# Kernel optimization log

Measured on AMD Instinct MI355X. Metric: run time of the kernel, lower is better.

The kernel has to match this reference:

```python
import jax, jax.numpy as jnp
import numpy as np
import math

HEADS = 4
DIM_HEAD = 32
EPS = 1e-5

def _ln_channels(x):
    # LayerNorm over channel axis (axis=1) of NCHW, no affine (eps=1e-5)
    mu = jnp.mean(x, axis=1, keepdims=True)
    var = jnp.mean((x - mu) ** 2, axis=1, keepdims=True)
    return (x - mu) * jax.lax.rsqrt(var + EPS)

def setup_inputs() -> dict:
    key = jax.random.key(0)
    k1, k2, k3, k4 = jax.random.split(key, 4)
    dim, inner = 256, HEADS * DIM_HEAD
    x = jax.random.normal(k1, (16, dim, 64, 64), dtype=jnp.float32)
    Wqkv = jax.random.normal(k2, (3 * inner, dim), dtype=jnp.float32) * (1.0 / math.sqrt(dim))
    Wout = jax.random.normal(k3, (dim, inner), dtype=jnp.float32) * (1.0 / math.sqrt(inner))
    bout = jax.random.normal(k4, (dim,), dtype=jnp.float32) * 0.01
    return {"x": x, "Wqkv": Wqkv, "Wout": Wout, "bout": bout}

def reference(x, Wqkv, Wout, bout):
    B, C, H, W = x.shape
    N = H * W
    inner = HEADS * DIM_HEAD
    # pre-norm (channel-wise LayerNorm via permute in torch)
    normed = _ln_channels(x)
    # 1x1 conv to qkv: [B, 3*inner, H, W]
    qkv = jnp.einsum('oc,bchw->bohw', Wqkv, normed)
    q, k, v = jnp.split(qkv, 3, axis=1)
    # [B, inner, H, W] -> [B, heads, N, dim_head]
    def to_heads(t):
        return t.reshape(B, HEADS, DIM_HEAD, N).transpose(0, 1, 3, 2)
    q, k, v = to_heads(q), to_heads(k), to_heads(v)
    q = jax.nn.softmax(q, axis=-1)          # over dim_head
    k = jax.nn.softmax(k, axis=-2)          # over N
    q = q / math.sqrt(DIM_HEAD)
    v = v / N
    context = jnp.einsum('bhnd,bhne->bhde', k, v)   # [B,h,d,d]
    out = jnp.einsum('bhde,bhnd->bhne', context, q) # [B,h,N,d]
    out = out.transpose(0, 1, 3, 2).reshape(B, inner, H, W)
    out = jnp.einsum('oc,bchw->bohw', Wout, out) + bout[None, :, None, None]
    out = _ln_channels(out)                  # LinearAttention.out_norm
    return out + x                           # residual
```

## Files before the change

### kernel.cpp

```cpp
#include <hip/hip_runtime.h>
#include <hip/hip_bf16.h>
#include <math.h>

#define BATCH 16
#define CH 256
#define NPOS 4096
#define INNER 128
#define HEADS 4
#define DH 32

typedef __hip_bfloat16 bf16;
typedef short bf8v __attribute__((ext_vector_type(8)));
typedef float f32x4 __attribute__((ext_vector_type(4)));

__device__ __forceinline__ float b2f(bf16 v) { return __bfloat162float(v); }
__device__ __forceinline__ float us2f(unsigned short u) {
    unsigned w = ((unsigned)u) << 16; float f; __builtin_memcpy(&f, &w, 4); return f;
}
__device__ __forceinline__ unsigned short f2us(float f) {
    bf16 h = __float2bfloat16(f); unsigned short u; __builtin_memcpy(&u, &h, 2); return u;
}
__device__ __forceinline__ bf16 f2b(float v) { return __float2bfloat16(v); }

__global__ __launch_bounds__(256)
void prep_w_kernel(const float* __restrict__ Wqkv, bf16* __restrict__ wqb,
                   float* __restrict__ wqs) {
    int idx = (blockIdx.x * 256 + threadIdx.x) * 4;
    float4 w = *(const float4*)&Wqkv[idx];
    ushort4 u;
    u.x = f2us(w.x); u.y = f2us(w.y); u.z = f2us(w.z); u.w = f2us(w.w);
    *(ushort4*)&wqb[idx] = u;
    float s4 = us2f(u.x) + us2f(u.y) + us2f(u.z) + us2f(u.w);
    #pragma unroll
    for (int m = 1; m <= 32; m <<= 1) s4 += __shfl_xor(s4, m, 64);
    if ((threadIdx.x & 63) == 0)
        wqs[blockIdx.x * 4 + (threadIdx.x >> 6)] = s4;
}

__global__ __launch_bounds__(256)
void fused_qkv_kernel(const float* __restrict__ x, const bf16* __restrict__ wqb,
                      const float* __restrict__ wqs,
                      bf16* __restrict__ p, float* __restrict__ ctxp) {
    __shared__ char smem[36864];
    __shared__ float stats[640];

    const int b = blockIdx.y, tile = blockIdx.x, n0 = tile * 64;
    const int tid = threadIdx.x;
    const int w = tid >> 6, lane = tid & 63;
    const int lrow = lane & 15, kq = lane >> 4;
    bf16* A = (bf16*)smem;

    {
        const int nq = tid & 15, cp = tid >> 4;
        float s[4] = {0.f,0.f,0.f,0.f}, sq[4] = {0.f,0.f,0.f,0.f};
        #pragma unroll
        for (int i = 0; i < 8; ++i) {
            int c0 = cp * 2 + 32 * i;
            const float* xp = x + ((size_t)b * CH + c0) * NPOS + n0 + nq * 4;
            float4 fa = *(const float4*)xp;
            float4 fb = *(const float4*)(xp + NPOS);
            #pragma unroll
            for (int j = 0; j < 4; ++j) {
                float va = (&fa.x)[j], vb = (&fb.x)[j];
                s[j] += va + vb; sq[j] += va * va + vb * vb;
                *(unsigned*)&A[(nq * 4 + j) * 264 + c0] =
                    (unsigned)f2us(va) | ((unsigned)f2us(vb) << 16);
            }
        }
        #pragma unroll
        for (int j = 0; j < 4; ++j) {
            s[j]  += __shfl_xor(s[j], 16, 64);  sq[j] += __shfl_xor(sq[j], 16, 64);
            s[j]  += __shfl_xor(s[j], 32, 64);  sq[j] += __shfl_xor(sq[j], 32, 64);
            if (lane < 16) {
                stats[(nq * 4 + j) * 8 + w * 2]     = s[j];
                stats[(nq * 4 + j) * 8 + w * 2 + 1] = sq[j];
            }
        }
    }
    __syncthreads();
    if (tid < 64) {
        float s  = stats[tid*8] + stats[tid*8+2] + stats[tid*8+4] + stats[tid*8+6];
        float sq = stats[tid*8+1] + stats[tid*8+3] + stats[tid*8+5] + stats[tid*8+7];
        float m = s * (1.f / 256.f);
        float var = sq * (1.f / 256.f) - m * m;
        stats[512 + tid * 2] = m;
        stats[512 + tid * 2 + 1] = rsqrtf(var + 1e-5f);
    }
    __syncthreads();

    ushort4 ekp[4][2];
    float se0 = 0.f, se1 = 0.f;

    for (int ph = 0; ph < 3; ++ph) {
        const bf16* wp = wqb + (size_t)(ph * 128 + w * 32) * 256;
        const float cs0 = wqs[ph * 128 + w * 32 + lrow];
        const float cs1 = wqs[ph * 128 + w * 32 + 16 + lrow];
        f32x4 acc[4][2];
        #pragma unroll
        for (int i = 0; i < 4; ++i) {
            acc[i][0] = (f32x4){0.f,0.f,0.f,0.f};
            acc[i][1] = (f32x4){0.f,0.f,0.f,0.f};
        }
        #pragma unroll 4
        for (int k0 = 0; k0 < 256; k0 += 32) {
            bf8v af[4], bfr[2];
            #pragma unroll
            for (int t = 0; t < 4; ++t)
                af[t] = *(const bf8v*)&A[(t * 16 + lrow) * 264 + k0 + kq * 8];
            #pragma unroll
            for (int t = 0; t < 2; ++t)
                bfr[t] = *(const bf8v*)&wp[(size_t)(t * 16 + lrow) * 256 + k0 + kq * 8];
            #pragma unroll
            for (int mt = 0; mt < 4; ++mt)
                #pragma unroll
                for (int nt = 0; nt < 2; ++nt)
                    acc[mt][nt] = __builtin_amdgcn_mfma_f32_16x16x32_bf16(
                        af[mt], bfr[nt], acc[mt][nt], 0, 0, 0);
        }

        if (ph == 0) {
            unsigned* pg32 = (unsigned*)p;
            #pragma unroll
            for (int mt = 0; mt < 4; ++mt)
                #pragma unroll
                for (int r = 0; r < 4; ++r) {
                    int row = mt * 16 + kq * 4 + r;
                    float mu = stats[512 + row * 2], rsn = stats[512 + row * 2 + 1];
                    float e0 = __expf(b2f(f2b((acc[mt][0][r] - mu * cs0) * rsn)));
                    float e1 = __expf(b2f(f2b((acc[mt][1][r] - mu * cs1) * rsn)));
                    float s = e0 + e1;
                    s += __shfl_xor(s, 1, 64);  s += __shfl_xor(s, 2, 64);
                    s += __shfl_xor(s, 4, 64);  s += __shfl_xor(s, 8, 64);
                    float rd = 1.f / s;
                    pg32[(size_t)(b * NPOS + n0 + row) * 64 + w * 16 + lrow] =
                        (unsigned)f2us(e0 * rd) | ((unsigned)f2us(e1 * rd) << 16);
                }
        } else if (ph == 1) {
            se0 = 0.f; se1 = 0.f;
            #pragma unroll
            for (int mt = 0; mt < 4; ++mt) {
                ushort4 u0, u1;
                unsigned short q_;
                #pragma unroll
                for (int r = 0; r < 4; ++r) {
                    int row = mt * 16 + kq * 4 + r;
                    float mu = stats[512 + row * 2], rsn = stats[512 + row * 2 + 1];
                    q_ = f2us(__expf(b2f(f2b((acc[mt][0][r] - mu * cs0) * rsn))));
                    se0 += us2f(q_); (&u0.x)[r] = q_;
                    q_ = f2us(__expf(b2f(f2b((acc[mt][1][r] - mu * cs1) * rsn))));
                    se1 += us2f(q_); (&u1.x)[r] = q_;
                }
                ekp[mt][0] = u0; ekp[mt][1] = u1;
            }
            se0 += __shfl_xor(se0, 16, 64); se0 += __shfl_xor(se0, 32, 64);
            se1 += __shfl_xor(se1, 16, 64); se1 += __shfl_xor(se1, 32, 64);
        } else {
            __syncthreads();
            bf16* ekt = (bf16*)(smem + w * 9216);
            bf16* vt  = (bf16*)(smem + w * 9216 + 4608);
            #pragma unroll
            for (int mt = 0; mt < 4; ++mt)
                #pragma unroll
                for (int nt = 0; nt < 2; ++nt) {
                    float csx = nt ? cs1 : cs0;
                    ushort4 vv;
                    #pragma unroll
                    for (int r = 0; r < 4; ++r) {
                        int row = mt * 16 + kq * 4 + r;
                        float mu = stats[512 + row * 2], rsn = stats[512 + row * 2 + 1];
                        (&vv.x)[r] = f2us((acc[mt][nt][r] - mu * csx) * rsn);
                    }
                    int d = nt * 16 + lrow, n = mt * 16 + kq * 4;
                    *(ushort4*)&vt[d * 72 + n]  = vv;
                    *(ushort4*)&ekt[d * 72 + n] = ekp[mt][nt];
                }
            f32x4 cacc[2][2];
            cacc[0][0] = (f32x4){0.f,0.f,0.f,0.f}; cacc[0][1] = cacc[0][0];
            cacc[1][0] = cacc[0][0];               cacc[1][1] = cacc[0][0];
            #pragma unroll
            for (int ks = 0; ks < 2; ++ks) {
                bf8v a2[2], bv2[2];
                a2[0]  = *(const bf8v*)&ekt[lrow * 72 + ks * 32 + kq * 8];
                a2[1]  = *(const bf8v*)&ekt[(16 + lrow) * 72 + ks * 32 + kq * 8];
                bv2[0] = *(const bf8v*)&vt[lrow * 72 + ks * 32 + kq * 8];
                bv2[1] = *(const bf8v*)&vt[(16 + lrow) * 72 + ks * 32 + kq * 8];
                #pragma unroll
                for (int mt2 = 0; mt2 < 2; ++mt2)
                    #pragma unroll
                    for (int nt2 = 0; nt2 < 2; ++nt2)
                        cacc[mt2][nt2] = __builtin_amdgcn_mfma_f32_16x16x32_bf16(
                            a2[mt2], bv2[nt2], cacc[mt2][nt2], 0, 0, 0);
            }
            float* pb = ctxp + ((size_t)(b * 64 + tile) * 4 + w) * 1056;
            #pragma unroll
            for (int mt2 = 0; mt2 < 2; ++mt2)
                #pragma unroll
                for (int nt2 = 0; nt2 < 2; ++nt2)
                    #pragma unroll
                    for (int r = 0; r < 4; ++r) {
                        int d = mt2 * 16 + kq * 4 + r, e = nt2 * 16 + lrow;
                        pb[d * 32 + e] = cacc[mt2][nt2][r];
                    }
            if (kq == 0) {
                pb[1024 + lrow] = se0;
                pb[1024 + 16 + lrow] = se1;
            }
        }
    }
}

__global__ __launch_bounds__(256)
void ctx_wmod_kernel(const float* __restrict__ ctxp, const float* __restrict__ Wout,
                     bf16* __restrict__ wmod) {
    __shared__ float cs[1056];
    int h = blockIdx.x, b = blockIdx.y, ch = blockIdx.z;
    int tid = threadIdx.x;

    #pragma unroll
    for (int i = 0; i < 2; ++i) {
        int s = i * 256 + tid;
        if (s < 264) {
            f32x4 a = (f32x4){0.f,0.f,0.f,0.f};
            const float* src = ctxp + (size_t)(b * 64 * 4 + h) * 1056 + s * 4;
            for (int t = 0; t < 64; ++t)
                a += *(const f32x4*)(src + (size_t)t * 4 * 1056);
            *(f32x4*)&cs[s * 4] = a;
        }
    }
    __syncthreads();

    int c = ch * 128 + (tid >> 1);
    int dh = tid & 1;
    const float* wr = Wout + (size_t)c * INNER + h * DH;
    float wv[32];
    #pragma unroll
    for (int i = 0; i < 8; ++i) {
        float4 t = *(const float4*)&wr[i * 4];
        wv[i * 4] = t.x; wv[i * 4 + 1] = t.y; wv[i * 4 + 2] = t.z; wv[i * 4 + 3] = t.w;
    }
    const float SCALE = 4.3158341e-05f;
    unsigned* wm32 = (unsigned*)(wmod + ((size_t)b * CH + c) * INNER + h * DH);
    #pragma unroll
    for (int dd = 0; dd < 8; ++dd) {
        int d1 = dh * 8 + dd, d2 = d1 + 16;
        const float* c1 = &cs[d1 * 32];
        const float* c2 = &cs[d2 * 32];
        float s1 = 0.f, s2 = 0.f;
        #pragma unroll
        for (int e4 = 0; e4 < 8; ++e4) {
            f32x4 t1 = *(const f32x4*)&c1[e4 * 4];
            f32x4 t2 = *(const f32x4*)&c2[e4 * 4];
            #pragma unroll
            for (int j = 0; j < 4; ++j) {
                s1 += wv[e4 * 4 + j] * t1[j];
                s2 += wv[e4 * 4 + j] * t2[j];
            }
        }
        float v1 = s1 * SCALE / cs[1024 + d1];
        float v2 = s2 * SCALE / cs[1024 + d2];
        wm32[d1] = (unsigned)f2us(v1) | ((unsigned)f2us(v2) << 16);
    }
}

__global__ __launch_bounds__(256)
void fused_out_kernel(const bf16* __restrict__ p, const bf16* __restrict__ wmod,
                      const float* __restrict__ bout, const float* __restrict__ x,
                      float* __restrict__ out) {
    __shared__ char lds[37376];
    bf16* Ap = (bf16*)lds;
    float* ct = (float*)lds;
    float* st = (float*)(lds + 34816);

    const int b = blockIdx.y, n0 = blockIdx.x * 64;
    const int tid = threadIdx.x;
    const int w = tid >> 6, lane = tid & 63;
    const int lrow = lane & 15, kq = lane >> 4;

    {
        const uint4* pg = (const uint4*)p;
        unsigned* A32 = (unsigned*)Ap;
        #pragma unroll
        for (int i = 0; i < 4; ++i) {
            int idx = i * 256 + tid;
            int c4 = idx & 15, n = idx >> 4;
            uint4 u = pg[(size_t)(b * NPOS + n0 + n) * 16 + c4];
            *(uint4*)(A32 + n * 68 + c4 * 4) = u;
        }
    }
    __syncthreads();

    f32x4 acc[4][4];
    #pragma unroll
    for (int i = 0; i < 4; ++i)
        #pragma unroll
        for (int j = 0; j < 4; ++j) acc[i][j] = (f32x4){0.f, 0.f, 0.f, 0.f};

    const bf16* wb = wmod + (size_t)b * CH * INNER + (size_t)(w * 64) * INNER;
    #pragma unroll 2
    for (int k0 = 0; k0 < 128; k0 += 32) {
        bf8v af[4], bfr[4];
        #pragma unroll
        for (int t = 0; t < 4; ++t)
            af[t] = *(const bf8v*)&Ap[(t * 16 + lrow) * 136 + k0 + kq * 8];
        #pragma unroll
        for (int t = 0; t < 4; ++t)
            bfr[t] = *(const bf8v*)&wb[(size_t)(t * 16 + lrow) * 128 + k0 + kq * 8];
        #pragma unroll
        for (int mt = 0; mt < 4; ++mt)
            #pragma unroll
            for (int nt = 0; nt < 4; ++nt)
                acc[mt][nt] = __builtin_amdgcn_mfma_f32_16x16x32_bf16(
                    af[mt], bfr[nt], acc[mt][nt], 0, 0, 0);
    }

    #pragma unroll
    for (int nt = 0; nt < 4; ++nt) {
        float bv = bout[w * 64 + nt * 16 + lrow];
        #pragma unroll
        for (int mt = 0; mt < 4; ++mt)
            #pragma unroll
            for (int r = 0; r < 4; ++r) acc[mt][nt][r] += bv;
    }

    #pragma unroll
    for (int mt = 0; mt < 4; ++mt)
        #pragma unroll
        for (int r = 0; r < 4; ++r) {
            float s = 0.f, sq = 0.f;
            #pragma unroll
            for (int nt = 0; nt < 4; ++nt) {
                float v = acc[mt][nt][r];
                s += v; sq += v * v;
            }
            #pragma unroll
            for (int m = 1; m <= 8; m <<= 1) {
                s += __shfl_xor(s, m, 64);
                sq += __shfl_xor(sq, m, 64);
            }
            if (lrow == 0) {
                int row = mt * 16 + kq * 4 + r;
                st[w * 128 + row * 2] = s;
                st[w * 128 + row * 2 + 1] = sq;
            }
        }
    __syncthreads();
    if (tid < 64) {
        float s  = st[tid * 2]       + st[128 + tid * 2]
                 + st[256 + tid * 2] + st[384 + tid * 2];
        float sq = st[tid * 2 + 1]       + st[128 + tid * 2 + 1]
                 + st[256 + tid * 2 + 1] + st[384 + tid * 2 + 1];
        float m = s * (1.f / 256.f);
        float var = sq * (1.f / 256.f) - m * m;
        st[512 + tid * 2] = m;
        st[512 + tid * 2 + 1] = rsqrtf(var + 1e-5f);
    }
    __syncthreads();
    #pragma unroll
    for (int mt = 0; mt < 4; ++mt)
        #pragma unroll
        for (int r = 0; r < 4; ++r) {
            int row = mt * 16 + kq * 4 + r;
            float m = st[512 + row * 2], rs = st[512 + row * 2 + 1];
            #pragma unroll
            for (int nt = 0; nt < 4; ++nt)
                acc[mt][nt][r] = (acc[mt][nt][r] - m) * rs;
        }

    #pragma unroll 1
    for (int pr = 0; pr < 2; ++pr) {
        __syncthreads();
        if ((w >> 1) == pr) {
            #pragma unroll
            for (int mt = 0; mt < 4; ++mt)
                #pragma unroll
                for (int nt = 0; nt < 4; ++nt)
                    #pragma unroll
                    for (int r = 0; r < 4; ++r)
                        ct[((w & 1) * 64 + nt * 16 + lrow) * 68 + mt * 16 + kq * 4 + r]
                            = acc[mt][nt][r];
        }
        __syncthreads();
        #pragma unroll
        for (int i = 0; i < 8; ++i) {
            int idx = i * 256 + tid;
            int n4 = (idx & 15) * 4, cl = idx >> 4;
            size_t gi = ((size_t)b * CH + pr * 128 + cl) * NPOS + n0 + n4;
            f32x4 cv = *(const f32x4*)&ct[cl * 68 + n4];
            f32x4 xv = *(const f32x4*)&x[gi];
            __builtin_nontemporal_store(cv + xv, (f32x4*)&out[gi]);
        }
    }
}

extern "C" void kernel_launch(void* const* d_in, const int* in_sizes, int n_in,
                              void* d_out, int out_size, void* d_ws, size_t ws_size,
                              hipStream_t stream) {
    const float* x    = (const float*)d_in[0];
    const float* Wqkv = (const float*)d_in[1];
    const float* Wout = (const float*)d_in[2];
    const float* bout = (const float*)d_in[3];
    float* out = (float*)d_out;

    char* ws = (char*)d_ws;
    bf16*  p      = (bf16*)ws;
    float* ctxp   = (float*)(ws + 16777216);
    bf16*  wmod   = (bf16*)(ws + 34349056);
    bf16*  wqb    = (bf16*)(ws + 35397632);
    float* wqs    = (float*)(ws + 35594240);

    prep_w_kernel<<<dim3(96), 256, 0, stream>>>(Wqkv, wqb, wqs);
    fused_qkv_kernel<<<dim3(64, BATCH), 256, 0, stream>>>(x, wqb, wqs, p, ctxp);
    ctx_wmod_kernel<<<dim3(HEADS, BATCH, 2), 256, 0, stream>>>(ctxp, Wout, wmod);
    fused_out_kernel<<<dim3(64, BATCH), 256, 0, stream>>>(p, wmod, bout, x, out);
}
```

Measured before the change: 187.6 us.

## Recompute softmaxed Q in output kernel instead of round-tripping through global memory

Q is no longer computed and stored to a global bf16 buffer in the QKV kernel. Instead, the output kernel reloads x, converts it to bf16 in LDS, and recomputes the Q projection with MFMA using per-position LayerNorm mean/rstd that the first kernel saved. This removes the 16 MB write and read of Q. In exchange it adds a second 64 MB fp32 read of x and extra matmul and exp work in the output kernel.

Result: no change. 188.7 us (+0.6%).

```diff
diff --git a/kernel.cpp b/kernel.cpp
--- a/kernel.cpp
+++ b/kernel.cpp
@@ -39,8 +39,8 @@
 
 __global__ __launch_bounds__(256)
 void fused_qkv_kernel(const float* __restrict__ x, const bf16* __restrict__ wqb,
-                      const float* __restrict__ wqs,
-                      bf16* __restrict__ p, float* __restrict__ ctxp) {
+                      const float* __restrict__ wqs, float* __restrict__ musr,
+                      float* __restrict__ ctxp) {
     __shared__ char smem[36864];
     __shared__ float stats[640];
 
@@ -85,13 +85,15 @@
         float var = sq * (1.f / 256.f) - m * m;
         stats[512 + tid * 2] = m;
         stats[512 + tid * 2 + 1] = rsqrtf(var + 1e-5f);
+        float2 ms; ms.x = m; ms.y = stats[512 + tid * 2 + 1];
+        *(float2*)&musr[((size_t)b * NPOS + n0 + tid) * 2] = ms;
     }
     __syncthreads();
 
     ushort4 ekp[4][2];
     float se0 = 0.f, se1 = 0.f;
 
-    for (int ph = 0; ph < 3; ++ph) {
+    for (int ph = 1; ph < 3; ++ph) {
         const bf16* wp = wqb + (size_t)(ph * 128 + w * 32) * 256;
         const float cs0 = wqs[ph * 128 + w * 32 + lrow];
         const float cs1 = wqs[ph * 128 + w * 32 + 16 + lrow];
@@ -118,24 +120,7 @@
                         af[mt], bfr[nt], acc[mt][nt], 0, 0, 0);
         }
 
-        if (ph == 0) {
-            unsigned* pg32 = (unsigned*)p;
-            #pragma unroll
-            for (int mt = 0; mt < 4; ++mt)
-                #pragma unroll
-                for (int r = 0; r < 4; ++r) {
-                    int row = mt * 16 + kq * 4 + r;
-                    float mu = stats[512 + row * 2], rsn = stats[512 + row * 2 + 1];
-                    float e0 = __expf(b2f(f2b((acc[mt][0][r] - mu * cs0) * rsn)));
-                    float e1 = __expf(b2f(f2b((acc[mt][1][r] - mu * cs1) * rsn)));
-                    float s = e0 + e1;
-                    s += __shfl_xor(s, 1, 64);  s += __shfl_xor(s, 2, 64);
-                    s += __shfl_xor(s, 4, 64);  s += __shfl_xor(s, 8, 64);
-                    float rd = 1.f / s;
-                    pg32[(size_t)(b * NPOS + n0 + row) * 64 + w * 16 + lrow] =
-                        (unsigned)f2us(e0 * rd) | ((unsigned)f2us(e1 * rd) << 16);
-                }
-        } else if (ph == 1) {
+        if (ph == 1) {
             se0 = 0.f; se1 = 0.f;
             #pragma unroll
             for (int mt = 0; mt < 4; ++mt) {
@@ -263,10 +248,13 @@
 }
 
 __global__ __launch_bounds__(256)
-void fused_out_kernel(const bf16* __restrict__ p, const bf16* __restrict__ wmod,
+void fused_out_kernel(const bf16* __restrict__ wqb, const float* __restrict__ wqs,
+                      const float* __restrict__ musr, const bf16* __restrict__ wmod,
                       const float* __restrict__ bout, const float* __restrict__ x,
                       float* __restrict__ out) {
     __shared__ char lds[37376];
+    bf16* A  = (bf16*)lds;
+    float* mus = (float*)(lds + 33792);
     bf16* Ap = (bf16*)lds;
     float* ct = (float*)lds;
     float* st = (float*)(lds + 34816);
@@ -277,15 +265,77 @@
     const int lrow = lane & 15, kq = lane >> 4;
 
     {
-        const uint4* pg = (const uint4*)p;
-        unsigned* A32 = (unsigned*)Ap;
+        const int nq = tid & 15, cp = tid >> 4;
+        #pragma unroll
+        for (int i = 0; i < 8; ++i) {
+            int c0 = cp * 2 + 32 * i;
+            const float* xp = x + ((size_t)b * CH + c0) * NPOS + n0 + nq * 4;
+            float4 fa = *(const float4*)xp;
+            float4 fb = *(const float4*)(xp + NPOS);
+            #pragma unroll
+            for (int j = 0; j < 4; ++j)
+                *(unsigned*)&A[(nq * 4 + j) * 264 + c0] =
+                    (unsigned)f2us((&fa.x)[j]) | ((unsigned)f2us((&fb.x)[j]) << 16);
+        }
+    }
+    if (tid < 64) {
+        float2 ms = *(const float2*)&musr[((size_t)b * NPOS + n0 + tid) * 2];
+        mus[tid * 2] = ms.x; mus[tid * 2 + 1] = ms.y;
+    }
+    __syncthreads();
+
+    unsigned ppack[4][4];
+    {
+        const bf16* wp = wqb + (size_t)(w * 32) * 256;
+        const float cs0 = wqs[w * 32 + lrow];
+        const float cs1 = wqs[w * 32 + 16 + lrow];
+        f32x4 qacc[4][2];
         #pragma unroll
         for (int i = 0; i < 4; ++i) {
-            int idx = i * 256 + tid;
-            int c4 = idx & 15, n = idx >> 4;
-            uint4 u = pg[(size_t)(b * NPOS + n0 + n) * 16 + c4];
-            *(uint4*)(A32 + n * 68 + c4 * 4) = u;
-        }
+            qacc[i][0] = (f32x4){0.f,0.f,0.f,0.f};
+            qacc[i][1] = (f32x4){0.f,0.f,0.f,0.f};
+        }
+        #pragma unroll 4
+        for (int k0 = 0; k0 < 256; k0 += 32) {
+            bf8v af[4], bfr[2];
+            #pragma unroll
+            for (int t = 0; t < 4; ++t)
+                af[t] = *(const bf8v*)&A[(t * 16 + lrow) * 264 + k0 + kq * 8];
+            #pragma unroll
+            for (int t = 0; t < 2; ++t)
+                bfr[t] = *(const bf8v*)&wp[(size_t)(t * 16 + lrow) * 256 + k0 + kq * 8];
+            #pragma unroll
+            for (int mt = 0; mt < 4; ++mt)
+                #pragma unroll
+                for (int nt = 0; nt < 2; ++nt)
+                    qacc[mt][nt] = __builtin_amdgcn_mfma_f32_16x16x32_bf16(
+                        af[mt], bfr[nt], qacc[mt][nt], 0, 0, 0);
+        }
+        #pragma unroll
+        for (int mt = 0; mt < 4; ++mt)
+            #pragma unroll
+            for (int r = 0; r < 4; ++r) {
+                int row = mt * 16 + kq * 4 + r;
+                float mu = mus[row * 2], rsn = mus[row * 2 + 1];
+                float e0 = __expf(b2f(f2b((qacc[mt][0][r] - mu * cs0) * rsn)));
+                float e1 = __expf(b2f(f2b((qacc[mt][1][r] - mu * cs1) * rsn)));
+                float s = e0 + e1;
+                s += __shfl_xor(s, 1, 64);  s += __shfl_xor(s, 2, 64);
+                s += __shfl_xor(s, 4, 64);  s += __shfl_xor(s, 8, 64);
+                float rd = 1.f / s;
+                ppack[mt][r] = (unsigned)f2us(e0 * rd) | ((unsigned)f2us(e1 * rd) << 16);
+            }
+    }
+    __syncthreads();
+    {
+        unsigned* Ap32 = (unsigned*)Ap;
+        #pragma unroll
+        for (int mt = 0; mt < 4; ++mt)
+            #pragma unroll
+            for (int r = 0; r < 4; ++r) {
+                int row = mt * 16 + kq * 4 + r;
+                Ap32[row * 68 + w * 16 + lrow] = ppack[mt][r];
+            }
     }
     __syncthreads();
 
@@ -402,14 +452,15 @@
     float* out = (float*)d_out;
 
     char* ws = (char*)d_ws;
-    bf16*  p      = (bf16*)ws;
-    float* ctxp   = (float*)(ws + 16777216);
-    bf16*  wmod   = (bf16*)(ws + 34349056);
-    bf16*  wqb    = (bf16*)(ws + 35397632);
-    float* wqs    = (float*)(ws + 35594240);
+    float* ctxp   = (float*)ws;
+    bf16*  wmod   = (bf16*)(ws + 17301504);
+    bf16*  wqb    = (bf16*)(ws + 18350080);
+    float* wqs    = (float*)(ws + 18546688);
+    float* musr   = (float*)(ws + 18548224);
 
     prep_w_kernel<<<dim3(96), 256, 0, stream>>>(Wqkv, wqb, wqs);
-    fused_qkv_kernel<<<dim3(64, BATCH), 256, 0, stream>>>(x, wqb, wqs, p, ctxp);
+    fused_qkv_kernel<<<dim3(64, BATCH), 256, 0, stream>>>(x, wqb, wqs, musr, ctxp);
     ctx_wmod_kernel<<<dim3(HEADS, BATCH, 2), 256, 0, stream>>>(ctxp, Wout, wmod);
-    fused_out_kernel<<<dim3(64, BATCH), 256, 0, stream>>>(p, wmod, bout, x, out);
-}
+    fused_out_kernel<<<dim3(64, BATCH), 256, 0, stream>>>(wqb, wqs, musr, wmod,
+                                                          bout, x, out);
+}
```
